# Kernel tuning notes

Measured on AMD Instinct MI355X. Metric: run time of the kernel, lower is better.

The kernel has to match this reference:

```python
import jax, jax.numpy as jnp
import numpy as np

B, S, D = 4, 16, 512          # batch, seq, attention_dim
V, T = 32000, 18              # vocab_size, tree_depth
INNER = V - 1                 # internal nodes of Huffman tree


def setup_inputs() -> dict:
    key = jax.random.key(0)
    k_att, k_w, k_idx, k_bit = jax.random.split(key, 4)
    att = jax.random.normal(k_att, (B, S, D), dtype=jnp.float32)
    weight = jax.random.normal(k_w, (INNER, D), dtype=jnp.float32) * 0.02
    path_index = jax.random.randint(k_idx, (V * T,), 0, INNER, dtype=jnp.int64)
    # left/right branch bits: sign=+1,bias=0 -> p ; sign=-1,bias=1 -> 1-p
    bits = jax.random.randint(k_bit, (V * T,), 0, 2).astype(jnp.float32)
    path_sign = 1.0 - 2.0 * bits
    path_bias = bits
    return {
        "att": att,
        "weight": weight,
        "path_index": path_index,
        "path_sign": path_sign,
        "path_bias": path_bias,
        "vocab_size": V,
        "tree_depth": T,
    }


def reference(att, weight, path_index, path_sign, path_bias, vocab_size, tree_depth):
    # h: sigmoid of linear projection onto internal-node vectors  [B,S,INNER]
    h = jax.nn.sigmoid(jnp.einsum("bsd,nd->bsn", att, weight))
    # gather per-(token,depth) internal-node probs, flip via sign/bias
    g = jnp.take(h, path_index, axis=-1) * path_sign + path_bias  # [B,S,V*T]
    Hm = g.reshape(att.shape[0], -1, vocab_size, tree_depth)      # [B,S,V,T]
    return jnp.sum(jnp.log(Hm), axis=-1)                          # [B,S,V]
```

## Files before the change

kernel.cpp:

```cpp
#include <hip/hip_runtime.h>

#define BS    64
#define DDIM  512
#define NV    32000
#define TD    18
#define INNER 31999

typedef __attribute__((ext_vector_type(8))) short short8;
typedef __attribute__((ext_vector_type(4))) float floatx4;

__device__ __forceinline__ float bf16_to_f32(unsigned short u) {
    union { unsigned int i; float f; } v; v.i = ((unsigned int)u) << 16; return v.f;
}
__device__ __forceinline__ unsigned short f32_to_bf16(float f) {
    union { float f; unsigned int i; } v; v.f = f;
    unsigned int r = v.i + 0x7FFFu + ((v.i >> 16) & 1u);
    return (unsigned short)(r >> 16);
}
__device__ __forceinline__ short8 cvt8(float4 a, float4 b) {
    short8 s;
    s[0] = (short)f32_to_bf16(a.x); s[1] = (short)f32_to_bf16(a.y);
    s[2] = (short)f32_to_bf16(a.z); s[3] = (short)f32_to_bf16(a.w);
    s[4] = (short)f32_to_bf16(b.x); s[5] = (short)f32_to_bf16(b.y);
    s[6] = (short)f32_to_bf16(b.z); s[7] = (short)f32_to_bf16(b.w);
    return s;
}

__global__ __launch_bounds__(256) void prep_att(
    const float4* __restrict__ att, ushort4* __restrict__ attb)
{
    int i = blockIdx.x * 256 + threadIdx.x;
    float4 a = att[i];
    ushort4 r;
    r.x = f32_to_bf16(a.x); r.y = f32_to_bf16(a.y);
    r.z = f32_to_bf16(a.z); r.w = f32_to_bf16(a.w);
    attb[i] = r;
}

#define LOADCH(BB, AA, c)                                                    \
    {                                                                        \
        _Pragma("unroll")                                                    \
        for (int s = 0; s < 4; ++s) {                                        \
            BB[2*s]   = *(const float4*)(bbase + (c)*128 + s*32);            \
            BB[2*s+1] = *(const float4*)(bbase + (c)*128 + s*32 + 4);        \
            AA[2*s]   = *(const short8*)(a0 + (c)*128 + s*32);               \
            AA[2*s+1] = *(const short8*)(a1 + (c)*128 + s*32);               \
        }                                                                    \
    }
#define COMPCH(BB, AA)                                                       \
    {                                                                        \
        _Pragma("unroll")                                                    \
        for (int s = 0; s < 4; ++s) {                                        \
            short8 bfrag = cvt8(BB[2*s], BB[2*s+1]);                         \
            acc0 = __builtin_amdgcn_mfma_f32_16x16x32_bf16(AA[2*s],   bfrag, acc0, 0, 0, 0); \
            acc1 = __builtin_amdgcn_mfma_f32_16x16x32_bf16(AA[2*s+1], bfrag, acc1, 0, 0, 0); \
        }                                                                    \
    }

__global__ __launch_bounds__(256) void gemm_logsig(
    const unsigned short* __restrict__ attb,
    const float* __restrict__ weight,
    unsigned int* __restrict__ pairsT)
{
    const int tid  = threadIdx.x;
    const int lane = tid & 63;
    const int wave = tid >> 6;
    const int nsub = wave & 1;
    const int msub = wave >> 1;
    const int l15  = lane & 15;
    const int quad = lane >> 4;
    const int B0   = blockIdx.x * 32;

    floatx4 acc0 = (floatx4){0.f, 0.f, 0.f, 0.f};
    floatx4 acc1 = (floatx4){0.f, 0.f, 0.f, 0.f};

    int brow = B0 + nsub * 16 + l15;
    if (brow > INNER - 1) brow = INNER - 1;
    const float*          bbase = weight + (size_t)brow * DDIM + quad * 8;
    const unsigned short* a0    = attb + (size_t)(msub * 32 + l15) * DDIM + quad * 8;
    const unsigned short* a1    = a0 + 16 * DDIM;

    float4 bufA[8], bufB[8];
    short8 afA[8], afB[8];

    LOADCH(bufA, afA, 0);
    LOADCH(bufB, afB, 1);
    COMPCH(bufA, afA);
    LOADCH(bufA, afA, 2);
    COMPCH(bufB, afB);
    LOADCH(bufB, afB, 3);
    COMPCH(bufA, afA);
    COMPCH(bufB, afB);

    const int n = B0 + nsub * 16 + l15;
    if (n < INNER) {
        unsigned int* dst = pairsT + ((size_t)n << 6) + msub * 32 + quad * 4;
        floatx4 accs[2] = {acc0, acc1};
#pragma unroll
        for (int mt = 0; mt < 2; ++mt) {
            unsigned int wds[4];
#pragma unroll
            for (int r = 0; r < 4; ++r) {
                float x = accs[mt][r];
                float lp = -(fmaxf(-x, 0.f) + __logf(1.f + __expf(-fabsf(x))));
                float lm = lp - x;
                wds[r] = (unsigned int)f32_to_bf16(lp)
                       | ((unsigned int)f32_to_bf16(lm) << 16);
            }
            uint4 wv; wv.x = wds[0]; wv.y = wds[1]; wv.z = wds[2]; wv.w = wds[3];
            *(uint4*)(dst + mt * 16) = wv;
        }
    }
}

__global__ __launch_bounds__(256) void gather_bs(
    const unsigned int* __restrict__ pairsT,
    const int* __restrict__ idx,
    const unsigned int* __restrict__ signbits,
    float* __restrict__ out)
{
    __shared__ unsigned int eLDS[576];
    __shared__ float tile[32][65];
    const int tid   = threadIdx.x;
    const int lane  = tid & 63;
    const int wave  = tid >> 6;
    const int vbase = blockIdx.x * 32;

    const unsigned int* w = (const unsigned int*)idx;
    bool i64 = true;
#pragma unroll
    for (int j = 1; j < 16; j += 2) i64 &= (w[j] == 0u);

    for (int q = tid; q < 576; q += 256) {
        int g = vbase * TD + q;
        int val = i64 ? idx[2 * g] : idx[g];
        eLDS[q] = ((unsigned int)val << 1) | (signbits[g] >> 31);
    }
    __syncthreads();

#pragma unroll
    for (int i = 0; i < 8; i += 2) {
        const int vA = wave * 8 + i;
        const int vB = vA + 1;
        const unsigned int* cA = eLDS + vA * TD;
        const unsigned int* cB = eLDS + vB * TD;
        unsigned int eA[TD], eB[TD], pA[TD], pB[TD];
#pragma unroll
        for (int t = 0; t < TD; ++t) { eA[t] = cA[t]; eB[t] = cB[t]; }
#pragma unroll
        for (int t = 0; t < TD; ++t) {
            pA[t] = pairsT[((size_t)(eA[t] >> 1) << 6) + lane];
            pB[t] = pairsT[((size_t)(eB[t] >> 1) << 6) + lane];
        }
        float sA = 0.f, sB = 0.f;
#pragma unroll
        for (int t = 0; t < TD; ++t) {
            sA += bf16_to_f32((unsigned short)(pA[t] >> ((eA[t] & 1u) << 4)));
            sB += bf16_to_f32((unsigned short)(pB[t] >> ((eB[t] & 1u) << 4)));
        }
        tile[vA][lane] = sA;
        tile[vB][lane] = sB;
    }
    __syncthreads();

    const int bs  = threadIdx.x >> 2;
    const int seg = threadIdx.x & 3;
    float4 r0, r1;
    r0.x = tile[seg * 8 + 0][bs]; r0.y = tile[seg * 8 + 1][bs];
    r0.z = tile[seg * 8 + 2][bs]; r0.w = tile[seg * 8 + 3][bs];
    r1.x = tile[seg * 8 + 4][bs]; r1.y = tile[seg * 8 + 5][bs];
    r1.z = tile[seg * 8 + 6][bs]; r1.w = tile[seg * 8 + 7][bs];
    float4* dst = (float4*)(out + (size_t)bs * NV + vbase + seg * 8);
    dst[0] = r0; dst[1] = r1;
}

extern "C" void kernel_launch(void* const* d_in, const int* in_sizes, int n_in,
                              void* d_out, int out_size, void* d_ws, size_t ws_size,
                              hipStream_t stream)
{
    const float*        att    = (const float*)d_in[0];
    const float*        weight = (const float*)d_in[1];
    const int*          pidx   = (const int*)d_in[2];
    const unsigned int* psign  = (const unsigned int*)d_in[3];
    float* out = (float*)d_out;

    char* ws = (char*)d_ws;
    unsigned int* pairsT = (unsigned int*)ws;
    ushort4*      attb   = (ushort4*)(ws + 8192000);

    prep_att<<<32, 256, 0, stream>>>((const float4*)att, attb);
    gemm_logsig<<<1000, 256, 0, stream>>>((const unsigned short*)attb, weight, pairsT);
    gather_bs<<<1000, 256, 0, stream>>>(pairsT, pidx, psign, out);
}
```

Baseline: 145.1 us.

## Fuse prep, GEMM and gather into one cooperative persistent kernel with grid sync

Replaces three launches with a single cooperative kernel of 256 persistent blocks. Each block converts the whole activation matrix to bf16 into swizzled LDS, loops over GEMM tiles, does a grid-wide sync, then loops over gather chunks. This removes two launch boundaries and the global round trip of the converted activations. In exchange every block redoes the activation conversion, LDS use grows to 64KB per block, which limits occupancy, and the grid sync adds its own cost. If the cooperative launch fails, two separate fallback kernels run instead.

```diff
diff --git a/kernel.cpp b/kernel.cpp
--- a/kernel.cpp
+++ b/kernel.cpp
@@ -1,10 +1,15 @@
 #include <hip/hip_runtime.h>
+#include <hip/hip_cooperative_groups.h>
+
+namespace cg = cooperative_groups;
 
 #define BS    64
 #define DDIM  512
 #define NV    32000
 #define TD    18
 #define INNER 31999
+#define NTILE 1000
+#define GRID  256
 
 typedef __attribute__((ext_vector_type(8))) short short8;
 typedef __attribute__((ext_vector_type(4))) float floatx4;
@@ -26,71 +31,67 @@
     return s;
 }
 
-__global__ __launch_bounds__(256) void prep_att(
-    const float4* __restrict__ att, ushort4* __restrict__ attb)
-{
-    int i = blockIdx.x * 256 + threadIdx.x;
-    float4 a = att[i];
-    ushort4 r;
-    r.x = f32_to_bf16(a.x); r.y = f32_to_bf16(a.y);
-    r.z = f32_to_bf16(a.z); r.w = f32_to_bf16(a.w);
-    attb[i] = r;
-}
-
-#define LOADCH(BB, AA, c)                                                    \
-    {                                                                        \
-        _Pragma("unroll")                                                    \
-        for (int s = 0; s < 4; ++s) {                                        \
-            BB[2*s]   = *(const float4*)(bbase + (c)*128 + s*32);            \
-            BB[2*s+1] = *(const float4*)(bbase + (c)*128 + s*32 + 4);        \
-            AA[2*s]   = *(const short8*)(a0 + (c)*128 + s*32);               \
-            AA[2*s+1] = *(const short8*)(a1 + (c)*128 + s*32);               \
-        }                                                                    \
-    }
-#define COMPCH(BB, AA)                                                       \
-    {                                                                        \
-        _Pragma("unroll")                                                    \
-        for (int s = 0; s < 4; ++s) {                                        \
-            short8 bfrag = cvt8(BB[2*s], BB[2*s+1]);                         \
-            acc0 = __builtin_amdgcn_mfma_f32_16x16x32_bf16(AA[2*s],   bfrag, acc0, 0, 0, 0); \
-            acc1 = __builtin_amdgcn_mfma_f32_16x16x32_bf16(AA[2*s+1], bfrag, acc1, 0, 0, 0); \
-        }                                                                    \
-    }
-
-__global__ __launch_bounds__(256) void gemm_logsig(
-    const unsigned short* __restrict__ attb,
-    const float* __restrict__ weight,
-    unsigned int* __restrict__ pairsT)
-{
-    const int tid  = threadIdx.x;
+__device__ __forceinline__ void stage_A(const float* __restrict__ att,
+                                        char* lds, int tid)
+{
+    const float4* a4 = (const float4*)att;
+    for (int it = 0; it < 32; ++it) {
+        int p = it * 256 + tid;
+        float4 a = a4[p];
+        int row = p >> 7;
+        int c8  = (p & 127) << 3;
+        ushort4 r;
+        r.x = f32_to_bf16(a.x); r.y = f32_to_bf16(a.y);
+        r.z = f32_to_bf16(a.z); r.w = f32_to_bf16(a.w);
+        *(ushort4*)(lds + row * 1024 + (c8 ^ ((row & 7) << 4))) = r;
+    }
+}
+
+__device__ __forceinline__ void gemm_tile(
+    const char* As, const float* __restrict__ weight,
+    unsigned int* __restrict__ pairsT, int tile, int tid)
+{
     const int lane = tid & 63;
     const int wave = tid >> 6;
     const int nsub = wave & 1;
     const int msub = wave >> 1;
     const int l15  = lane & 15;
     const int quad = lane >> 4;
-    const int B0   = blockIdx.x * 32;
+    const int B0   = tile * 32;
+
+    int brow = B0 + nsub * 16 + l15;
+    if (brow > INNER - 1) brow = INNER - 1;
+    const float* bbase = weight + (size_t)brow * DDIM + quad * 8;
+
+    const int   r0    = msub * 32 + l15;
+    const int   sw    = (r0 & 7) << 4;
+    const char* arow0 = As + r0 * 1024;
+    const char* arow1 = arow0 + 16 * 1024;
+    const int   cbq   = quad * 16;
 
     floatx4 acc0 = (floatx4){0.f, 0.f, 0.f, 0.f};
     floatx4 acc1 = (floatx4){0.f, 0.f, 0.f, 0.f};
-
-    int brow = B0 + nsub * 16 + l15;
-    if (brow > INNER - 1) brow = INNER - 1;
-    const float*          bbase = weight + (size_t)brow * DDIM + quad * 8;
-    const unsigned short* a0    = attb + (size_t)(msub * 32 + l15) * DDIM + quad * 8;
-    const unsigned short* a1    = a0 + 16 * DDIM;
-
-    float4 bufA[8], bufB[8];
-    short8 afA[8], afB[8];
-
-    LOADCH(bufA, afA, 0);
-    LOADCH(bufB, afB, 1);
-    COMPCH(bufA, afA);
-    LOADCH(bufA, afA, 2);
-    COMPCH(bufB, afB);
-    LOADCH(bufB, afB, 3);
-    COMPCH(bufA, afA);
-    COMPCH(bufB, afB);
+    float4 bA[8], bB[8];
+
+#define LB(BUF, c) { _Pragma("unroll")                                        \
+    for (int s = 0; s < 4; ++s) {                                             \
+        BUF[2*s]   = *(const float4*)(bbase + (c)*128 + s*32);                \
+        BUF[2*s+1] = *(const float4*)(bbase + (c)*128 + s*32 + 4); } }
+#define CB(BUF, c) { _Pragma("unroll")                                        \
+    for (int s = 0; s < 4; ++s) {                                             \
+        short8 bf = cvt8(BUF[2*s], BUF[2*s+1]);                               \
+        int cb = ((c)*256 + s*64 + cbq) ^ sw;                                 \
+        short8 af0 = *(const short8*)(arow0 + cb);                            \
+        short8 af1 = *(const short8*)(arow1 + cb);                            \
+        acc0 = __builtin_amdgcn_mfma_f32_16x16x32_bf16(af0, bf, acc0, 0,0,0); \
+        acc1 = __builtin_amdgcn_mfma_f32_16x16x32_bf16(af1, bf, acc1, 0,0,0); } }
+
+    LB(bA, 0); LB(bB, 1);
+    CB(bA, 0); LB(bA, 2);
+    CB(bB, 1); LB(bB, 3);
+    CB(bA, 2); CB(bB, 3);
+#undef LB
+#undef CB
 
     const int n = B0 + nsub * 16 + l15;
     if (n < INNER) {
@@ -113,24 +114,18 @@
     }
 }
 
-__global__ __launch_bounds__(256) void gather_bs(
+__device__ __forceinline__ void gather_chunk(
     const unsigned int* __restrict__ pairsT,
-    const int* __restrict__ idx,
-    const unsigned int* __restrict__ signbits,
-    float* __restrict__ out)
-{
-    __shared__ unsigned int eLDS[576];
-    __shared__ float tile[32][65];
-    const int tid   = threadIdx.x;
+    const int* __restrict__ idx, const unsigned int* __restrict__ signbits,
+    float* __restrict__ out, char* lds, int chunk, int tid, bool i64)
+{
+    unsigned int* eLDS = (unsigned int*)lds;
+    float (*tp)[65]    = (float(*)[65])(lds + 2304);
     const int lane  = tid & 63;
     const int wave  = tid >> 6;
-    const int vbase = blockIdx.x * 32;
-
-    const unsigned int* w = (const unsigned int*)idx;
-    bool i64 = true;
-#pragma unroll
-    for (int j = 1; j < 16; j += 2) i64 &= (w[j] == 0u);
-
+    const int vbase = chunk * 32;
+
+    __syncthreads();
     for (int q = tid; q < 576; q += 256) {
         int g = vbase * TD + q;
         int val = i64 ? idx[2 * g] : idx[g];
@@ -158,20 +153,69 @@
             sA += bf16_to_f32((unsigned short)(pA[t] >> ((eA[t] & 1u) << 4)));
             sB += bf16_to_f32((unsigned short)(pB[t] >> ((eB[t] & 1u) << 4)));
         }
-        tile[vA][lane] = sA;
-        tile[vB][lane] = sB;
-    }
-    __syncthreads();
-
-    const int bs  = threadIdx.x >> 2;
-    const int seg = threadIdx.x & 3;
+        tp[vA][lane] = sA;
+        tp[vB][lane] = sB;
+    }
+    __syncthreads();
+
+    const int bs  = tid >> 2;
+    const int seg = tid & 3;
     float4 r0, r1;
-    r0.x = tile[seg * 8 + 0][bs]; r0.y = tile[seg * 8 + 1][bs];
-    r0.z = tile[seg * 8 + 2][bs]; r0.w = tile[seg * 8 + 3][bs];
-    r1.x = tile[seg * 8 + 4][bs]; r1.y = tile[seg * 8 + 5][bs];
-    r1.z = tile[seg * 8 + 6][bs]; r1.w = tile[seg * 8 + 7][bs];
+    r0.x = tp[seg * 8 + 0][bs]; r0.y = tp[seg * 8 + 1][bs];
+    r0.z = tp[seg * 8 + 2][bs]; r0.w = tp[seg * 8 + 3][bs];
+    r1.x = tp[seg * 8 + 4][bs]; r1.y = tp[seg * 8 + 5][bs];
+    r1.z = tp[seg * 8 + 6][bs]; r1.w = tp[seg * 8 + 7][bs];
     float4* dst = (float4*)(out + (size_t)bs * NV + vbase + seg * 8);
     dst[0] = r0; dst[1] = r1;
+}
+
+__device__ __forceinline__ bool idx_is_i64(const int* idx) {
+    const unsigned int* w = (const unsigned int*)idx;
+    bool i64 = true;
+#pragma unroll
+    for (int j = 1; j < 16; j += 2) i64 &= (w[j] == 0u);
+    return i64;
+}
+
+__global__ __launch_bounds__(256) void fused(
+    const float* __restrict__ att, const float* __restrict__ weight,
+    unsigned int* __restrict__ pairsT,
+    const int* __restrict__ idx, const unsigned int* __restrict__ signbits,
+    float* __restrict__ out)
+{
+    __shared__ __align__(16) char lds[65536];
+    const int tid = threadIdx.x;
+    const int bid = blockIdx.x;
+
+    stage_A(att, lds, tid);
+    __syncthreads();
+    for (int tile = bid; tile < NTILE; tile += GRID)
+        gemm_tile(lds, weight, pairsT, tile, tid);
+
+    cg::this_grid().sync();
+
+    const bool i64 = idx_is_i64(idx);
+    for (int chunk = bid; chunk < NTILE; chunk += GRID)
+        gather_chunk(pairsT, idx, signbits, out, lds, chunk, tid, i64);
+}
+
+__global__ __launch_bounds__(256) void k_gemm(
+    const float* __restrict__ att, const float* __restrict__ weight,
+    unsigned int* __restrict__ pairsT)
+{
+    __shared__ __align__(16) char lds[65536];
+    stage_A(att, lds, threadIdx.x);
+    __syncthreads();
+    gemm_tile(lds, weight, pairsT, blockIdx.x, threadIdx.x);
+}
+__global__ __launch_bounds__(256) void k_gather(
+    const unsigned int* __restrict__ pairsT,
+    const int* __restrict__ idx, const unsigned int* __restrict__ signbits,
+    float* __restrict__ out)
+{
+    __shared__ __align__(16) char lds[16384];
+    const bool i64 = idx_is_i64(idx);
+    gather_chunk(pairsT, idx, signbits, out, lds, blockIdx.x, threadIdx.x, i64);
 }
 
 extern "C" void kernel_launch(void* const* d_in, const int* in_sizes, int n_in,
@@ -184,11 +228,14 @@
     const unsigned int* psign  = (const unsigned int*)d_in[3];
     float* out = (float*)d_out;
 
-    char* ws = (char*)d_ws;
-    unsigned int* pairsT = (unsigned int*)ws;
-    ushort4*      attb   = (ushort4*)(ws + 8192000);
-
-    prep_att<<<32, 256, 0, stream>>>((const float4*)att, attb);
-    gemm_logsig<<<1000, 256, 0, stream>>>((const unsigned short*)attb, weight, pairsT);
-    gather_bs<<<1000, 256, 0, stream>>>(pairsT, pidx, psign, out);
-}
+    unsigned int* pairsT = (unsigned int*)d_ws;
+
+    void* kargs[] = { (void*)&att, (void*)&weight, (void*)&pairsT,
+                      (void*)&pidx, (void*)&psign, (void*)&out };
+    hipError_t err = hipLaunchCooperativeKernel(
+        (const void*)fused, dim3(GRID), dim3(256), kargs, 0, stream);
+    if (err != hipSuccess) {
+        k_gemm  <<<NTILE, 256, 0, stream>>>(att, weight, pairsT);
+        k_gather<<<NTILE, 256, 0, stream>>>(pairsT, pidx, psign, out);
+    }
+}
```

After: 202.7 us. +39.6%, slower.
